# Kernel tuning notes

Hardware: AMD Instinct MI355X
Metric: run time of the kernel (lower is better)

## Reference

```python
import jax, jax.numpy as jnp
import numpy as np

# Contiguous token segment lengths per group (static, sums to 4096)
LEN_GROUPS = (256, 512, 768, 384, 640, 512, 576, 448)
NUM_GROUPS, D_IN, D_OUT = 8, 512, 512
BATCH = 16


def setup_inputs() -> dict:
    key = jax.random.key(0)
    k1, k2, k3 = jax.random.split(key, 3)
    T = int(sum(LEN_GROUPS))
    x = jax.random.normal(k1, (BATCH, T, D_IN), dtype=jnp.float32)
    # nn.Linear default init: U(-1/sqrt(fan_in), 1/sqrt(fan_in))
    bound = 1.0 / np.sqrt(D_IN)
    W = jax.random.uniform(k2, (NUM_GROUPS, D_OUT, D_IN), jnp.float32, -bound, bound)
    b = jax.random.uniform(k3, (NUM_GROUPS, D_OUT), jnp.float32, -bound, bound)
    return {"x": x, "W": W, "b": b}


def reference(x, W, b):
    # Per-group Linear over contiguous token segments, then concat along tokens.
    # Loop is over a small static group count; segment bounds are Python ints,
    # so slicing is static and jit-compatible.
    outs = []
    start = 0
    for i, L in enumerate(LEN_GROUPS):
        seg = x[:, start:start + L]                     # [B, L, D_in]
        outs.append(jnp.einsum('btd,od->bto', seg, W[i]) + b[i])  # [B, L, D_out]
        start += L
    return jnp.concatenate(outs, axis=1)               # [B, T, D_out]
```

## Files before the change

kernel.cpp:

```cpp
#include <hip/hip_runtime.h>
#include <hip/hip_bf16.h>
#include <cstdint>

#define BATCH 16
#define TTOT  4096
#define DIN   512
#define DOUT  512
#define NG    8
#define NJOB  33
#define NKT   8

typedef float f32x4 __attribute__((ext_vector_type(4)));
typedef short s16x4 __attribute__((ext_vector_type(4)));
typedef short s16x8 __attribute__((ext_vector_type(8)));

__device__ __forceinline__ short f2b(float f) {
    union { __bf16 b; short s; } u; u.b = (__bf16)f; return u.s;
}

__device__ __constant__ short JT0[NJOB] = {
    0,128, 256,384,512,640, 768,896,1024,1152,1280,1408, 1536,1664,1792,
    1920,2048,2176,2304,2432, 2560,2688,2816,2944, 3072,3200,3328,3456,
    3584, 3648, 3712,3840,3968};
__device__ __constant__ char JG[NJOB] = {
    0,0, 1,1,1,1, 2,2,2,2,2,2, 3,3,3, 4,4,4,4,4, 5,5,5,5, 6,6,6,6, 6, 7, 7,7,7};
__device__ __constant__ char JBM[NJOB] = {
    127,127, 127,127,127,127, 127,127,127,127,127,127, 127,127,127,
    127,127,127,127,127, 127,127,127,127, 127,127,127,127, 63, 63, 127,127,127};

__global__ void wconv_kernel(const float* __restrict__ W, ushort* __restrict__ wbf) {
    int gid = blockIdx.x * 256 + threadIdx.x;
    int c = gid >> 10;
    int q = (gid & 1023) << 4;
    int row = q >> 7;
    int bc  = q & 127;
    int kbyte = bc ^ ((row & 7) << 4);
    int kt = c & 7, nt = (c >> 3) & 3, g = c >> 5;
    const float* wp = W + ((size_t)(g * DOUT + nt * 128 + row)) * DIN
                        + kt * 64 + (kbyte >> 1);
    float4 v0 = *reinterpret_cast<const float4*>(wp);
    float4 v1 = *reinterpret_cast<const float4*>(wp + 4);
    s16x8 o;
    o[0]=f2b(v0.x); o[1]=f2b(v0.y); o[2]=f2b(v0.z); o[3]=f2b(v0.w);
    o[4]=f2b(v1.x); o[5]=f2b(v1.y); o[6]=f2b(v1.z); o[7]=f2b(v1.w);
    *reinterpret_cast<s16x8*>((char*)wbf + (size_t)c * 16384 + q) = o;
}

__launch_bounds__(512, 4)
__global__ void gemm_kernel(const float* __restrict__ x,
                            const ushort* __restrict__ wbf,
                            const float* __restrict__ bias,
                            float* __restrict__ out) {
    __shared__ __align__(16) char smem[81920];

    const int tid  = threadIdx.x;
    const int lane = tid & 63;
    const int wv   = tid >> 6;
    const int wm   = wv >> 2;
    const int wn   = wv & 3;

    const int p    = blockIdx.x;
    const int l    = (p & 7) * 264 + (p >> 3);
    const int nt   = l & 3;
    const int rest = l >> 2;
    const int bbat = rest / NJOB;
    const int job  = rest - bbat * NJOB;
    const int t0   = JT0[job];
    const int g    = JG[job];
    const int bmm1 = JBM[job];
    const int n0   = nt << 7;

    const float* xbase = x + ((size_t)(bbat * TTOT + t0)) * DIN;
    const char*  bchunk = (const char*)wbf + (size_t)((g * 4 + nt) * 8) * 16384;

    char* abufs = smem;
    char* bring = smem + 32768;

    const int arow0 = (wv << 4) + (lane >> 4);
    const int col16 = lane & 15;
    const float* aptr = xbase + (size_t)arow0 * DIN + (col16 << 2);

    float4 aR0[4], aR1[4];

    f32x4 acc[4][2];
#pragma unroll
    for (int mi = 0; mi < 4; ++mi)
#pragma unroll
        for (int ni = 0; ni < 2; ++ni)
            acc[mi][ni] = (f32x4){0.f, 0.f, 0.f, 0.f};

#define ISSUE_A(j)                                                          \
    if ((j) < NKT) {                                                        \
        const float* s_ = aptr + ((j) << 6);                                \
        if (((j) & 1) == 0) {                                               \
            aR0[0] = *(const float4*)(s_);                                  \
            aR0[1] = *(const float4*)(s_ + 4 * DIN);                        \
            aR0[2] = *(const float4*)(s_ + 8 * DIN);                        \
            aR0[3] = *(const float4*)(s_ + 12 * DIN);                       \
        } else {                                                            \
            aR1[0] = *(const float4*)(s_);                                  \
            aR1[1] = *(const float4*)(s_ + 4 * DIN);                        \
            aR1[2] = *(const float4*)(s_ + 8 * DIN);                        \
            aR1[3] = *(const float4*)(s_ + 12 * DIN);                       \
        }                                                                   \
    }

#define ISSUE_B(j)                                                          \
    if ((j) < NKT) {                                                        \
        const char* src_ = bchunk + (size_t)(j) * 16384 + tid * 16;         \
        char* dst_ = bring + ((j) % 3) * 16384 + (wv << 10);                \
        __builtin_amdgcn_global_load_lds(                                   \
            (const __attribute__((address_space(1))) void*)src_,            \
            (__attribute__((address_space(3))) void*)dst_, 16, 0, 0);       \
        __builtin_amdgcn_global_load_lds(                                   \
            (const __attribute__((address_space(1))) void*)(src_ + 8192),   \
            (__attribute__((address_space(3))) void*)(dst_ + 8192), 16, 0, 0);\
    }

#define CVT_WRITE_A(j)                                                      \
    if ((j) < NKT) {                                                        \
        char* ab_ = abufs + ((j) & 1) * 16384;                              \
        _Pragma("unroll")                                                   \
        for (int r_ = 0; r_ < 4; ++r_) {                                    \
            float4 v_ = (((j) & 1) == 0) ? aR0[r_] : aR1[r_];               \
            s16x4 o_;                                                       \
            o_[0]=f2b(v_.x); o_[1]=f2b(v_.y); o_[2]=f2b(v_.z); o_[3]=f2b(v_.w);\
            int row_ = arow0 + r_ * 4;                                      \
            *(s16x4*)(ab_ + (row_ << 7) + (((col16 << 3)) ^ ((row_ & 7) << 4))) = o_; \
        }                                                                   \
    }

    const int colf = lane & 15;
    const int kg   = lane >> 4;

#define COMPUTE(j)                                                          \
    {                                                                       \
        const char* ab_ = abufs + ((j) & 1) * 16384;                        \
        const char* bb_ = bring + ((j) % 3) * 16384;                        \
        _Pragma("unroll")                                                   \
        for (int ks = 0; ks < 2; ++ks) {                                    \
            const int kb = ks * 64 + kg * 16;                               \
            s16x8 af[4], bf[2];                                             \
            _Pragma("unroll")                                               \
            for (int mi = 0; mi < 4; ++mi) {                                \
                int r_ = wm * 64 + mi * 16 + colf;                          \
                af[mi] = *(const s16x8*)(ab_ + (r_ << 7) + (kb ^ ((r_ & 7) << 4))); \
            }                                                               \
            _Pragma("unroll")                                               \
            for (int ni = 0; ni < 2; ++ni) {                                \
                int r_ = wn * 32 + ni * 16 + colf;                          \
                bf[ni] = *(const s16x8*)(bb_ + (r_ << 7) + (kb ^ ((r_ & 7) << 4))); \
            }                                                               \
            _Pragma("unroll")                                               \
            for (int mi = 0; mi < 4; ++mi)                                  \
                _Pragma("unroll")                                           \
                for (int ni = 0; ni < 2; ++ni)                              \
                    acc[mi][ni] = __builtin_amdgcn_mfma_f32_16x16x32_bf16(  \
                        af[mi], bf[ni], acc[mi][ni], 0, 0, 0);              \
        }                                                                   \
    }

#define FENCE asm volatile("" ::: "memory")
#define WAITV6 asm volatile("s_waitcnt vmcnt(6)" ::: "memory")
#define WAITV0 asm volatile("s_waitcnt vmcnt(0)" ::: "memory")
#define WAITL0 asm volatile("s_waitcnt lgkmcnt(0)" ::: "memory")
#define BARRIER do { FENCE; __builtin_amdgcn_s_barrier(); FENCE; } while (0)

    ISSUE_A(0); ISSUE_B(0);
    FENCE;
    ISSUE_A(1); ISSUE_B(1);
    FENCE;
    CVT_WRITE_A(0);
    WAITV6;
    WAITL0;
    BARRIER;

#pragma unroll
    for (int kt = 0; kt < NKT; ++kt) {
        ISSUE_A(kt + 2); ISSUE_B(kt + 2);
        FENCE;
        COMPUTE(kt);
        if (kt + 1 < NKT) {
            CVT_WRITE_A(kt + 1);
            if (kt + 2 < NKT) { WAITV6; }
            else              { WAITV0; }
            WAITL0;
            BARRIER;
        }
    }

    WAITL0;
    BARRIER;

    float* cbuf = (float*)smem;
#pragma unroll
    for (int mi = 0; mi < 4; ++mi)
#pragma unroll
        for (int ni = 0; ni < 2; ++ni) {
            int r0 = wm * 64 + mi * 16 + kg * 4;
            int c  = wn * 32 + ni * 16 + colf;
            f32x4 v = acc[mi][ni];
            cbuf[(r0 + 0) * 132 + c] = v[0];
            cbuf[(r0 + 1) * 132 + c] = v[1];
            cbuf[(r0 + 2) * 132 + c] = v[2];
            cbuf[(r0 + 3) * 132 + c] = v[3];
        }
    WAITL0;
    BARRIER;

    const int rr = tid >> 5;
    const int cc = (tid & 31) << 2;
    float4 bv = *reinterpret_cast<const float4*>(bias + (g << 9) + n0 + cc);
#pragma unroll
    for (int it = 0; it < 8; ++it) {
        int row = it * 16 + rr;
        if (row <= bmm1) {
            float4 v = *reinterpret_cast<const float4*>(cbuf + row * 132 + cc);
            float4 o4; o4.x = v.x + bv.x; o4.y = v.y + bv.y;
                       o4.z = v.z + bv.z; o4.w = v.w + bv.w;
            *reinterpret_cast<float4*>(
                out + ((size_t)(bbat * TTOT + t0 + row)) * DOUT + n0 + cc) = o4;
        }
    }
#undef ISSUE_A
#undef ISSUE_B
#undef CVT_WRITE_A
#undef COMPUTE
#undef FENCE
#undef WAITV6
#undef WAITV0
#undef WAITL0
#undef BARRIER
}

__launch_bounds__(256)
__global__ void gemm_fallback(const float* __restrict__ x,
                              const float* __restrict__ W,
                              const float* __restrict__ bias,
                              float* __restrict__ out) {
    __shared__ __align__(16) char smem[49152];
    const int tid  = threadIdx.x;
    const int lane = tid & 63;
    const int wid  = tid >> 6;
    const int wm   = wid >> 1;
    const int wn   = wid & 1;
    const int p  = blockIdx.x;
    const int l  = ((p & 7) << 9) + (p >> 3);
    const int mt = l >> 2;
    const int nt = l & 3;
    const int bb = mt >> 6;
    const int t0 = (mt & 63) << 6;
    const int n0 = nt << 7;
    int g = 0;
    if (t0 >= 256)  g++; if (t0 >= 768)  g++; if (t0 >= 1536) g++;
    if (t0 >= 1920) g++; if (t0 >= 2560) g++; if (t0 >= 3072) g++;
    if (t0 >= 3648) g++;
    const int arow = tid >> 2;
    const int acol = (tid & 3) << 4;
    const float* aptr = x + ((size_t)(bb * TTOT + t0 + arow)) * DIN + acol;
    float4 a0, a1, a2, a3;
    float4 bw0[4], bw1[4];
    auto load_global = [&](int k0) {
        a0 = *(const float4*)(aptr + k0);
        a1 = *(const float4*)(aptr + k0 + 4);
        a2 = *(const float4*)(aptr + k0 + 8);
        a3 = *(const float4*)(aptr + k0 + 12);
#pragma unroll
        for (int pp = 0; pp < 4; ++pp) {
            int idx = pp * 256 + tid;
            int row = idx >> 3, seg = idx & 7;
            const float* wp = W + ((size_t)((g << 9) + n0 + row)) * DIN + k0 + (seg << 3);
            bw0[pp] = *(const float4*)(wp);
            bw1[pp] = *(const float4*)(wp + 4);
        }
    };
    auto swz = [](int row, int bc) { return (row << 7) + (bc ^ ((row & 7) << 4)); };
    auto write_lds = [&](int buf) {
        char* ab  = smem + buf * 8192;
        char* bb_ = smem + 16384 + buf * 16384;
        s16x8 w0, w1;
        w0[0]=f2b(a0.x); w0[1]=f2b(a0.y); w0[2]=f2b(a0.z); w0[3]=f2b(a0.w);
        w0[4]=f2b(a1.x); w0[5]=f2b(a1.y); w0[6]=f2b(a1.z); w0[7]=f2b(a1.w);
        w1[0]=f2b(a2.x); w1[1]=f2b(a2.y); w1[2]=f2b(a2.z); w1[3]=f2b(a2.w);
        w1[4]=f2b(a3.x); w1[5]=f2b(a3.y); w1[6]=f2b(a3.z); w1[7]=f2b(a3.w);
        const int abase = acol << 1;
        *(s16x8*)(ab + swz(arow, abase))      = w0;
        *(s16x8*)(ab + swz(arow, abase + 16)) = w1;
#pragma unroll
        for (int pp = 0; pp < 4; ++pp) {
            int idx = pp * 256 + tid;
            int row = idx >> 3, seg = idx & 7;
            s16x8 wv;
            wv[0]=f2b(bw0[pp].x); wv[1]=f2b(bw0[pp].y);
            wv[2]=f2b(bw0[pp].z); wv[3]=f2b(bw0[pp].w);
            wv[4]=f2b(bw1[pp].x); wv[5]=f2b(bw1[pp].y);
            wv[6]=f2b(bw1[pp].z); wv[7]=f2b(bw1[pp].w);
            *(s16x8*)(bb_ + swz(row, seg << 4)) = wv;
        }
    };
    f32x4 acc[2][4];
#pragma unroll
    for (int mi = 0; mi < 2; ++mi)
#pragma unroll
        for (int ni = 0; ni < 4; ++ni) acc[mi][ni] = (f32x4){0.f,0.f,0.f,0.f};
    const int colf = lane & 15;
    const int kgrp = lane >> 4;
    auto compute = [&](int buf) {
        const char* ab  = smem + buf * 8192;
        const char* bb_ = smem + 16384 + buf * 16384;
#pragma unroll
        for (int ks = 0; ks < 2; ++ks) {
            const int kb = ks * 64 + kgrp * 16;
            s16x8 af[2], bf[4];
#pragma unroll
            for (int mi = 0; mi < 2; ++mi)
                af[mi] = *(const s16x8*)(ab + swz(wm * 32 + mi * 16 + colf, kb));
#pragma unroll
            for (int ni = 0; ni < 4; ++ni)
                bf[ni] = *(const s16x8*)(bb_ + swz(wn * 64 + ni * 16 + colf, kb));
#pragma unroll
            for (int mi = 0; mi < 2; ++mi)
#pragma unroll
                for (int ni = 0; ni < 4; ++ni)
                    acc[mi][ni] = __builtin_amdgcn_mfma_f32_16x16x32_bf16(
                        af[mi], bf[ni], acc[mi][ni], 0, 0, 0);
        }
    };
    load_global(0);
    write_lds(0);
    __syncthreads();
    int buf = 0;
#pragma unroll 1
    for (int kt = 0; kt < 8; ++kt) {
        if (kt < 7) load_global((kt + 1) << 6);
        compute(buf);
        if (kt < 7) write_lds(buf ^ 1);
        __syncthreads();
        buf ^= 1;
    }
    float* cbuf = (float*)smem;
    const int rowg = lane >> 4;
#pragma unroll
    for (int ni = 0; ni < 4; ++ni) {
        const int c = wn * 64 + ni * 16 + colf;
#pragma unroll
        for (int mi = 0; mi < 2; ++mi) {
            const int r = wm * 32 + mi * 16 + rowg * 4;
            f32x4 v = acc[mi][ni];
            cbuf[(r + 0) * 132 + c] = v[0];
            cbuf[(r + 1) * 132 + c] = v[1];
            cbuf[(r + 2) * 132 + c] = v[2];
            cbuf[(r + 3) * 132 + c] = v[3];
        }
    }
    __syncthreads();
    const int rr = tid >> 5;
    const int cc = (tid & 31) << 2;
    const float4 bv = *(const float4*)(bias + (g << 9) + n0 + cc);
#pragma unroll
    for (int it = 0; it < 8; ++it) {
        const int row = it * 8 + rr;
        float4 v = *(const float4*)(cbuf + row * 132 + cc);
        float4 o4; o4.x = v.x + bv.x; o4.y = v.y + bv.y;
                   o4.z = v.z + bv.z; o4.w = v.w + bv.w;
        *(float4*)(out + ((size_t)(bb * TTOT) + t0 + row) * DOUT + n0 + cc) = o4;
    }
}

extern "C" void kernel_launch(void* const* d_in, const int* in_sizes, int n_in,
                              void* d_out, int out_size, void* d_ws, size_t ws_size,
                              hipStream_t stream) {
    const float* x    = (const float*)d_in[0];
    const float* W    = (const float*)d_in[1];
    const float* bias = (const float*)d_in[2];
    float* out = (float*)d_out;

    const size_t wbytes = (size_t)NG * DOUT * DIN * sizeof(ushort);

    if (ws_size >= wbytes) {
        ushort* wbf = (ushort*)d_ws;
        wconv_kernel<<<1024, 256, 0, stream>>>(W, wbf);
        gemm_kernel<<<BATCH * NJOB * 4, 512, 0, stream>>>(x, wbf, bias, out);
    } else {
        gemm_fallback<<<BATCH * 64 * 4, 256, 0, stream>>>(x, W, bias, out);
    }
}
```

Baseline: 97.01 us.

## Use 256-thread blocks with 64x64 per-wave tiles and reorder block-to-job mapping

Halves the block to 4 waves, each computing a 64x64 output sub-tile (4x4 MFMA accumulators) instead of 64x32. This raises register reuse of A and B fragments per LDS read. A staging now uses 8-float loads per row packed into 16-byte LDS writes, and B loads issue 4 global-to-LDS transfers per thread. The block index decode changes so batch varies fastest within a job, aiming for better weight locality in cache. Fewer waves per CU and higher register pressure may reduce latency hiding.

```diff
diff --git a/kernel.cpp b/kernel.cpp
--- a/kernel.cpp
+++ b/kernel.cpp
@@ -11,7 +11,6 @@
 #define NKT   8
 
 typedef float f32x4 __attribute__((ext_vector_type(4)));
-typedef short s16x4 __attribute__((ext_vector_type(4)));
 typedef short s16x8 __attribute__((ext_vector_type(8)));
 
 __device__ __forceinline__ short f2b(float f) {
@@ -46,7 +45,7 @@
     *reinterpret_cast<s16x8*>((char*)wbf + (size_t)c * 16384 + q) = o;
 }
 
-__launch_bounds__(512, 4)
+__launch_bounds__(256, 2)
 __global__ void gemm_kernel(const float* __restrict__ x,
                             const ushort* __restrict__ wbf,
                             const float* __restrict__ bias,
@@ -56,149 +55,142 @@
     const int tid  = threadIdx.x;
     const int lane = tid & 63;
     const int wv   = tid >> 6;
-    const int wm   = wv >> 2;
-    const int wn   = wv & 3;
+    const int wm   = wv >> 1;
+    const int wn   = wv & 1;
+    const int colf = lane & 15;
+    const int kg   = lane >> 4;
 
     const int p    = blockIdx.x;
     const int l    = (p & 7) * 264 + (p >> 3);
     const int nt   = l & 3;
     const int rest = l >> 2;
-    const int bbat = rest / NJOB;
-    const int job  = rest - bbat * NJOB;
+    const int job  = rest >> 4;
+    const int bb   = rest & 15;
     const int t0   = JT0[job];
     const int g    = JG[job];
     const int bmm1 = JBM[job];
     const int n0   = nt << 7;
 
-    const float* xbase = x + ((size_t)(bbat * TTOT + t0)) * DIN;
-    const char*  bchunk = (const char*)wbf + (size_t)((g * 4 + nt) * 8) * 16384;
+    const char* bchunk = (const char*)wbf + (size_t)((g * 4 + nt) * 8) * 16384;
 
     char* abufs = smem;
     char* bring = smem + 32768;
 
-    const int arow0 = (wv << 4) + (lane >> 4);
-    const int col16 = lane & 15;
-    const float* aptr = xbase + (size_t)arow0 * DIN + (col16 << 2);
-
-    float4 aR0[4], aR1[4];
-
-    f32x4 acc[4][2];
-#pragma unroll
-    for (int mi = 0; mi < 4; ++mi)
-#pragma unroll
-        for (int ni = 0; ni < 2; ++ni)
-            acc[mi][ni] = (f32x4){0.f, 0.f, 0.f, 0.f};
-
-#define ISSUE_A(j)                                                          \
-    if ((j) < NKT) {                                                        \
-        const float* s_ = aptr + ((j) << 6);                                \
-        if (((j) & 1) == 0) {                                               \
-            aR0[0] = *(const float4*)(s_);                                  \
-            aR0[1] = *(const float4*)(s_ + 4 * DIN);                        \
-            aR0[2] = *(const float4*)(s_ + 8 * DIN);                        \
-            aR0[3] = *(const float4*)(s_ + 12 * DIN);                       \
-        } else {                                                            \
-            aR1[0] = *(const float4*)(s_);                                  \
-            aR1[1] = *(const float4*)(s_ + 4 * DIN);                        \
-            aR1[2] = *(const float4*)(s_ + 8 * DIN);                        \
-            aR1[3] = *(const float4*)(s_ + 12 * DIN);                       \
+    const int arow_s = (wv << 5) + (lane >> 3);
+    const int col8   = (lane & 7) << 3;
+    const float* aptr = x + ((size_t)(bb * TTOT + t0 + arow_s)) * DIN + col8;
+
+    float4 stE[4][2], stO[4][2];
+
+#define ISSUE_A(S, KT_) do {                                                \
+        _Pragma("unroll")                                                   \
+        for (int j_ = 0; j_ < 4; ++j_) {                                    \
+            const float* p_ = aptr + (size_t)(j_ * 8) * DIN + ((KT_) << 6); \
+            st##S[j_][0] = *(const float4*)(p_);                            \
+            st##S[j_][1] = *(const float4*)(p_ + 4);                        \
         }                                                                   \
-    }
-
-#define ISSUE_B(j)                                                          \
-    if ((j) < NKT) {                                                        \
-        const char* src_ = bchunk + (size_t)(j) * 16384 + tid * 16;         \
-        char* dst_ = bring + ((j) % 3) * 16384 + (wv << 10);                \
-        __builtin_amdgcn_global_load_lds(                                   \
-            (const __attribute__((address_space(1))) void*)src_,            \
-            (__attribute__((address_space(3))) void*)dst_, 16, 0, 0);       \
-        __builtin_amdgcn_global_load_lds(                                   \
-            (const __attribute__((address_space(1))) void*)(src_ + 8192),   \
-            (__attribute__((address_space(3))) void*)(dst_ + 8192), 16, 0, 0);\
-    }
-
-#define CVT_WRITE_A(j)                                                      \
-    if ((j) < NKT) {                                                        \
-        char* ab_ = abufs + ((j) & 1) * 16384;                              \
+    } while (0)
+
+#define ISSUE_B(KT_) do {                                                   \
+        const char* src_ = bchunk + (size_t)(KT_) * 16384 + tid * 16;       \
+        char* dst_ = bring + ((KT_) % 3) * 16384 + tid * 16;                \
         _Pragma("unroll")                                                   \
-        for (int r_ = 0; r_ < 4; ++r_) {                                    \
-            float4 v_ = (((j) & 1) == 0) ? aR0[r_] : aR1[r_];               \
-            s16x4 o_;                                                       \
-            o_[0]=f2b(v_.x); o_[1]=f2b(v_.y); o_[2]=f2b(v_.z); o_[3]=f2b(v_.w);\
-            int row_ = arow0 + r_ * 4;                                      \
-            *(s16x4*)(ab_ + (row_ << 7) + (((col16 << 3)) ^ ((row_ & 7) << 4))) = o_; \
+        for (int i_ = 0; i_ < 4; ++i_) {                                    \
+            __builtin_amdgcn_global_load_lds(                               \
+                (const __attribute__((address_space(1))) void*)(src_ + i_ * 4096), \
+                (__attribute__((address_space(3))) void*)(dst_ + i_ * 4096),\
+                16, 0, 0);                                                  \
         }                                                                   \
-    }
-
-    const int colf = lane & 15;
-    const int kg   = lane >> 4;
-
-#define COMPUTE(j)                                                          \
-    {                                                                       \
-        const char* ab_ = abufs + ((j) & 1) * 16384;                        \
-        const char* bb_ = bring + ((j) % 3) * 16384;                        \
+    } while (0)
+
+#define CVT_WRITE_A(S, KT_) do {                                            \
+        char* ab_ = abufs + ((KT_) & 1) * 16384;                            \
+        _Pragma("unroll")                                                   \
+        for (int j_ = 0; j_ < 4; ++j_) {                                    \
+            float4 lo_ = st##S[j_][0], hi_ = st##S[j_][1];                  \
+            s16x8 o_;                                                       \
+            o_[0]=f2b(lo_.x); o_[1]=f2b(lo_.y); o_[2]=f2b(lo_.z); o_[3]=f2b(lo_.w); \
+            o_[4]=f2b(hi_.x); o_[5]=f2b(hi_.y); o_[6]=f2b(hi_.z); o_[7]=f2b(hi_.w); \
+            int row_ = arow_s + j_ * 8;                                     \
+            int bc_ = (col8 << 1) ^ ((row_ & 7) << 4);                      \
+            *(s16x8*)(ab_ + (row_ << 7) + bc_) = o_;                        \
+        }                                                                   \
+    } while (0)
+
+#define COMPUTE(KT_) do {                                                   \
+        const char* ab_ = abufs + ((KT_) & 1) * 16384;                      \
+        const char* bb_ = bring + ((KT_) % 3) * 16384;                      \
         _Pragma("unroll")                                                   \
         for (int ks = 0; ks < 2; ++ks) {                                    \
-            const int kb = ks * 64 + kg * 16;                               \
-            s16x8 af[4], bf[2];                                             \
+            const int kb = ks * 64 + (kg << 4);                             \
+            s16x8 af[4], bf[4];                                             \
             _Pragma("unroll")                                               \
             for (int mi = 0; mi < 4; ++mi) {                                \
                 int r_ = wm * 64 + mi * 16 + colf;                          \
                 af[mi] = *(const s16x8*)(ab_ + (r_ << 7) + (kb ^ ((r_ & 7) << 4))); \
             }                                                               \
             _Pragma("unroll")                                               \
-            for (int ni = 0; ni < 2; ++ni) {                                \
-                int r_ = wn * 32 + ni * 16 + colf;                          \
+            for (int ni = 0; ni < 4; ++ni) {                                \
+                int r_ = wn * 64 + ni * 16 + colf;                          \
                 bf[ni] = *(const s16x8*)(bb_ + (r_ << 7) + (kb ^ ((r_ & 7) << 4))); \
             }                                                               \
             _Pragma("unroll")                                               \
             for (int mi = 0; mi < 4; ++mi)                                  \
                 _Pragma("unroll")                                           \
-                for (int ni = 0; ni < 2; ++ni)                              \
+                for (int ni = 0; ni < 4; ++ni)                              \
                     acc[mi][ni] = __builtin_amdgcn_mfma_f32_16x16x32_bf16(  \
                         af[mi], bf[ni], acc[mi][ni], 0, 0, 0);              \
         }                                                                   \
-    }
-
-#define FENCE asm volatile("" ::: "memory")
-#define WAITV6 asm volatile("s_waitcnt vmcnt(6)" ::: "memory")
-#define WAITV0 asm volatile("s_waitcnt vmcnt(0)" ::: "memory")
-#define WAITL0 asm volatile("s_waitcnt lgkmcnt(0)" ::: "memory")
+    } while (0)
+
+#define FENCE   asm volatile("" ::: "memory")
+#define WAITV12 asm volatile("s_waitcnt vmcnt(12)" ::: "memory")
+#define WAITV0  asm volatile("s_waitcnt vmcnt(0)" ::: "memory")
+#define WAITL0  asm volatile("s_waitcnt lgkmcnt(0)" ::: "memory")
 #define BARRIER do { FENCE; __builtin_amdgcn_s_barrier(); FENCE; } while (0)
 
-    ISSUE_A(0); ISSUE_B(0);
+    f32x4 acc[4][4];
+#pragma unroll
+    for (int mi = 0; mi < 4; ++mi)
+#pragma unroll
+        for (int ni = 0; ni < 4; ++ni)
+            acc[mi][ni] = (f32x4){0.f, 0.f, 0.f, 0.f};
+
+    ISSUE_A(E, 0); ISSUE_B(0);
     FENCE;
-    ISSUE_A(1); ISSUE_B(1);
+    ISSUE_A(O, 1); ISSUE_B(1);
     FENCE;
-    CVT_WRITE_A(0);
-    WAITV6;
+    CVT_WRITE_A(E, 0);
+    WAITV12;
     WAITL0;
     BARRIER;
 
 #pragma unroll
     for (int kt = 0; kt < NKT; ++kt) {
-        ISSUE_A(kt + 2); ISSUE_B(kt + 2);
-        FENCE;
+        if (kt + 2 < NKT) {
+            if (((kt) & 1) == 0) { ISSUE_A(E, kt + 2); } else { ISSUE_A(O, kt + 2); }
+            ISSUE_B(kt + 2);
+            FENCE;
+        }
         COMPUTE(kt);
         if (kt + 1 < NKT) {
-            CVT_WRITE_A(kt + 1);
-            if (kt + 2 < NKT) { WAITV6; }
-            else              { WAITV0; }
+            if (((kt + 1) & 1) == 0) { CVT_WRITE_A(E, kt + 1); }
+            else                     { CVT_WRITE_A(O, kt + 1); }
+            if (kt + 2 < NKT) { WAITV12; }
+            else              { WAITV0;  }
             WAITL0;
             BARRIER;
         }
     }
-
-    WAITL0;
     BARRIER;
 
     float* cbuf = (float*)smem;
 #pragma unroll
     for (int mi = 0; mi < 4; ++mi)
 #pragma unroll
-        for (int ni = 0; ni < 2; ++ni) {
+        for (int ni = 0; ni < 4; ++ni) {
             int r0 = wm * 64 + mi * 16 + kg * 4;
-            int c  = wn * 32 + ni * 16 + colf;
+            int c  = wn * 64 + ni * 16 + colf;
             f32x4 v = acc[mi][ni];
             cbuf[(r0 + 0) * 132 + c] = v[0];
             cbuf[(r0 + 1) * 132 + c] = v[1];
@@ -212,14 +204,14 @@
     const int cc = (tid & 31) << 2;
     float4 bv = *reinterpret_cast<const float4*>(bias + (g << 9) + n0 + cc);
 #pragma unroll
-    for (int it = 0; it < 8; ++it) {
-        int row = it * 16 + rr;
+    for (int it = 0; it < 16; ++it) {
+        int row = it * 8 + rr;
         if (row <= bmm1) {
             float4 v = *reinterpret_cast<const float4*>(cbuf + row * 132 + cc);
             float4 o4; o4.x = v.x + bv.x; o4.y = v.y + bv.y;
                        o4.z = v.z + bv.z; o4.w = v.w + bv.w;
             *reinterpret_cast<float4*>(
-                out + ((size_t)(bbat * TTOT + t0 + row)) * DOUT + n0 + cc) = o4;
+                out + ((size_t)(bb * TTOT + t0 + row)) * DOUT + n0 + cc) = o4;
         }
     }
 #undef ISSUE_A
@@ -227,7 +219,7 @@
 #undef CVT_WRITE_A
 #undef COMPUTE
 #undef FENCE
-#undef WAITV6
+#undef WAITV12
 #undef WAITV0
 #undef WAITL0
 #undef BARRIER
@@ -283,19 +275,19 @@
         w0[4]=f2b(a1.x); w0[5]=f2b(a1.y); w0[6]=f2b(a1.z); w0[7]=f2b(a1.w);
         w1[0]=f2b(a2.x); w1[1]=f2b(a2.y); w1[2]=f2b(a2.z); w1[3]=f2b(a2.w);
         w1[4]=f2b(a3.x); w1[5]=f2b(a3.y); w1[6]=f2b(a3.z); w1[7]=f2b(a3.w);
-        const int abase = acol << 1;
-        *(s16x8*)(ab + swz(arow, abase))      = w0;
-        *(s16x8*)(ab + swz(arow, abase + 16)) = w1;
+        const int abase2 = acol << 1;
+        *(s16x8*)(ab + swz(arow, abase2))      = w0;
+        *(s16x8*)(ab + swz(arow, abase2 + 16)) = w1;
 #pragma unroll
         for (int pp = 0; pp < 4; ++pp) {
             int idx = pp * 256 + tid;
             int row = idx >> 3, seg = idx & 7;
-            s16x8 wv;
-            wv[0]=f2b(bw0[pp].x); wv[1]=f2b(bw0[pp].y);
-            wv[2]=f2b(bw0[pp].z); wv[3]=f2b(bw0[pp].w);
-            wv[4]=f2b(bw1[pp].x); wv[5]=f2b(bw1[pp].y);
-            wv[6]=f2b(bw1[pp].z); wv[7]=f2b(bw1[pp].w);
-            *(s16x8*)(bb_ + swz(row, seg << 4)) = wv;
+            s16x8 wvv;
+            wvv[0]=f2b(bw0[pp].x); wvv[1]=f2b(bw0[pp].y);
+            wvv[2]=f2b(bw0[pp].z); wvv[3]=f2b(bw0[pp].w);
+            wvv[4]=f2b(bw1[pp].x); wvv[5]=f2b(bw1[pp].y);
+            wvv[6]=f2b(bw1[pp].z); wvv[7]=f2b(bw1[pp].w);
+            *(s16x8*)(bb_ + swz(row, seg << 4)) = wvv;
         }
     };
     f32x4 acc[2][4];
@@ -339,13 +331,12 @@
         buf ^= 1;
     }
     float* cbuf = (float*)smem;
-    const int rowg = lane >> 4;
 #pragma unroll
     for (int ni = 0; ni < 4; ++ni) {
         const int c = wn * 64 + ni * 16 + colf;
 #pragma unroll
         for (int mi = 0; mi < 2; ++mi) {
-            const int r = wm * 32 + mi * 16 + rowg * 4;
+            const int r = wm * 32 + mi * 16 + kgrp * 4;
             f32x4 v = acc[mi][ni];
             cbuf[(r + 0) * 132 + c] = v[0];
             cbuf[(r + 1) * 132 + c] = v[1];
@@ -380,7 +371,7 @@
     if (ws_size >= wbytes) {
         ushort* wbf = (ushort*)d_ws;
         wconv_kernel<<<1024, 256, 0, stream>>>(W, wbf);
-        gemm_kernel<<<BATCH * NJOB * 4, 512, 0, stream>>>(x, wbf, bias, out);
+        gemm_kernel<<<NJOB * BATCH * 4, 256, 0, stream>>>(x, wbf, bias, out);
     } else {
         gemm_fallback<<<BATCH * 64 * 4, 256, 0, stream>>>(x, W, bias, out);
     }
```

Result: no change. 95.62 us (-1.4%).
